# Optimization experiments

Measured on AMD Instinct MI355X. Metric: run time of the kernel, lower is better.

## Reference

```python
import jax, jax.numpy as jnp
import numpy as np

E, K, IN_DIM, OUT_DIM = 100000, 16, 128, 128


def _linear_init(key, out_d, in_d):
    kw, kb = jax.random.split(key)
    bound = 1.0 / np.sqrt(in_d)
    W = jax.random.uniform(kw, (out_d, in_d), minval=-bound, maxval=bound, dtype=jnp.float32)
    b = jax.random.uniform(kb, (out_d,), minval=-bound, maxval=bound, dtype=jnp.float32)
    return W, b


def setup_inputs() -> dict:
    key = jax.random.key(0)
    k_feat, k_adj, k1, k2, k3, k4 = jax.random.split(key, 6)
    edge_features = jax.random.normal(k_feat, (E, IN_DIM), dtype=jnp.float32)
    edge_adjacency = jax.random.randint(k_adj, (E, K), 0, E, dtype=jnp.int64)
    mW1, mb1 = _linear_init(k1, OUT_DIM, 2 * IN_DIM)
    mW2, mb2 = _linear_init(k2, OUT_DIM, OUT_DIM)
    uW1, ub1 = _linear_init(k3, OUT_DIM, IN_DIM + OUT_DIM)
    uW2, ub2 = _linear_init(k4, OUT_DIM, OUT_DIM)
    return {"edge_features": edge_features, "edge_adjacency": edge_adjacency,
            "mW1": mW1, "mb1": mb1, "mW2": mW2, "mb2": mb2,
            "uW1": uW1, "ub1": ub1, "uW2": ub2 * 0 + ub2 if False else uW1 * 0 + uW1 if False else uW1, "ub1_": ub1} if False else {
            "edge_features": edge_features, "edge_adjacency": edge_adjacency,
            "mW1": mW1, "mb1": mb1, "mW2": mW2, "mb2": mb2,
            "uW1": uW1, "ub1": ub1, "uW2": uW2, "ub2": ub2}


def reference(edge_features, edge_adjacency, mW1, mb1, mW2, mb2, uW1, ub1, uW2, ub2):
    D = edge_features.shape[1]
    # message_net first Linear on concat([feat_i, feat_j]) split into two halves
    # to avoid materializing the [E, K, 2D] concat tensor.
    Wi, Wj = mW1[:, :D], mW1[:, D:]                      # each [O, D]
    self_part = edge_features @ Wi.T                     # [E, O]
    nbr_feat = edge_features[edge_adjacency]             # [E, K, D] gather
    h = jax.nn.relu(self_part[:, None, :] + jnp.einsum('ekd,od->eko', nbr_feat, Wj) + mb1)
    msg = jnp.einsum('eko,po->ekp', h, mW2) + mb2        # [E, K, O]
    msg = msg.mean(axis=1)                               # mean over neighbors -> [E, O]
    # update_net on concat([feat_i, msg_i]), split likewise
    Ui, Um = uW1[:, :D], uW1[:, D:]
    u = jax.nn.relu(edge_features @ Ui.T + msg @ Um.T + ub1)
    return u @ uW2.T + ub2                               # [E, O]
```

## Files before the change

kernel.cpp:

```cpp
#include <hip/hip_runtime.h>
#include <hip/hip_bf16.h>

#define NE 100000
#define NK 16
#define ND 128
#define NTILES 6250

typedef __bf16 bf16_t;
typedef bf16_t bf16x8 __attribute__((ext_vector_type(8)));
typedef bf16_t bf16x4 __attribute__((ext_vector_type(4)));
typedef float f32x4 __attribute__((ext_vector_type(4)));
typedef float f32x2 __attribute__((ext_vector_type(2)));
typedef unsigned short u16;
typedef unsigned char u8;

__device__ __forceinline__ u16 f2bf(float f) {
  bf16_t h = (bf16_t)f;
  return __builtin_bit_cast(u16, h);
}

__global__ void k_prep(const float* __restrict__ mW1, const float* __restrict__ uW1,
                       const float* __restrict__ uW2, const float* __restrict__ mW2,
                       const float* __restrict__ ub1, const float* __restrict__ mb2,
                       u16* __restrict__ Wi_b, u16* __restrict__ Wj_b,
                       u16* __restrict__ Ui_b, u16* __restrict__ Wp_b,
                       u16* __restrict__ W2_b, float* __restrict__ bp)
{
  const int o = blockIdx.x, t = threadIdx.x;
  Wi_b[o * ND + t] = f2bf(mW1[o * 256 + t]);
  Wj_b[o * ND + t] = f2bf(mW1[o * 256 + 128 + t]);
  Ui_b[o * ND + t] = f2bf(uW1[o * 256 + t]);
  W2_b[o * ND + t] = f2bf(uW2[o * ND + t]);
  float acc = 0.f;
  for (int p = 0; p < 128; ++p)
    acc += uW1[o * 256 + 128 + p] * mW2[p * 128 + t];
  Wp_b[o * ND + t] = f2bf(acc);
  if (t == 0) {
    float b = ub1[o];
    for (int p = 0; p < 128; ++p) b += uW1[o * 256 + 128 + p] * mb2[p];
    bp[o] = b;
  }
}

__global__ __launch_bounds__(512) void k1_szt(
    const float* __restrict__ X, const u16* __restrict__ Wi_b,
    const u16* __restrict__ Wj_b, const u16* __restrict__ Ui_b,
    const float* __restrict__ mb1, const float* __restrict__ bp,
    u16* __restrict__ Sb, u8* __restrict__ Zf8, u16* __restrict__ T1)
{
  __shared__ u16 xt[16 * ND];
  __shared__ u16 eS[16 * ND];
  __shared__ u8  eZ[16 * ND];
  __shared__ u16 eT[16 * ND];
  const int tid = threadIdx.x, wid = tid >> 6, lane = tid & 63;
  const int r = lane & 15, q = lane >> 4;

  bf16x8 wiF[4], wjF[4], uiF[4];
  f32x4 mbF, bpF;
  {
    const int row = wid * 16 + r;
#pragma unroll
    for (int kk = 0; kk < 4; ++kk) {
      wiF[kk] = *(const bf16x8*)(Wi_b + row * ND + kk * 32 + q * 8);
      wjF[kk] = *(const bf16x8*)(Wj_b + row * ND + kk * 32 + q * 8);
      uiF[kk] = *(const bf16x8*)(Ui_b + row * ND + kk * 32 + q * 8);
    }
    mbF = *(const f32x4*)(mb1 + wid * 16 + q * 4);
    bpF = *(const f32x4*)(bp  + wid * 16 + q * 4);
  }

  const int rs = tid >> 5, cs = tid & 31;
  const int stb = rs * 256 + ((((cs >> 1) ^ (rs & 15)) << 4) | ((cs & 1) << 3));

  const int ewb = r * 256 + ((((wid * 2 + (q >> 1)) ^ (r & 15)) << 4) | ((q & 1) << 3));
  const int ezb = r * 128 + (((wid ^ (r & 7)) << 4) | (q * 4));
  const int erow = tid >> 5, c8 = tid & 31;
  const int erb = erow * 256 + ((((c8 >> 1) ^ (erow & 15)) << 4) | ((c8 & 1) << 3));
  const int zrb = erow * 128 + ((((c8 >> 2) ^ (erow & 7)) << 4) | ((c8 & 3) << 2));

  const long stride = gridDim.x;
  long t = blockIdx.x;
  if (t >= NTILES) return;

  f32x4 xr;
  auto gload = [&](long tt) {
    xr = *(const f32x4*)(X + (tt * 16 + rs) * ND + cs * 4);
  };
  auto stage = [&]() {
    bf16x4 b;
#pragma unroll
    for (int i = 0; i < 4; ++i) b[i] = (bf16_t)xr[i];
    *(bf16x4*)((char*)xt + stb) = b;
  };

  gload(t);
  stage();
  __syncthreads();

  for (; t < NTILES; t += stride) {
    const long tn = t + stride;
    if (tn < NTILES) gload(tn);

    bf16x8 xf[4];
#pragma unroll
    for (int kk = 0; kk < 4; ++kk)
      xf[kk] = *(const bf16x8*)((const char*)xt +
               r * 256 + (((kk * 4 + q) ^ (r & 15)) << 4));

    f32x4 aS = {0.f, 0.f, 0.f, 0.f};
    f32x4 aZ = {0.f, 0.f, 0.f, 0.f};
    f32x4 aT = {0.f, 0.f, 0.f, 0.f};
#pragma unroll
    for (int kk = 0; kk < 4; ++kk) {
      aS = __builtin_amdgcn_mfma_f32_16x16x32_bf16(wiF[kk], xf[kk], aS, 0, 0, 0);
      aZ = __builtin_amdgcn_mfma_f32_16x16x32_bf16(wjF[kk], xf[kk], aZ, 0, 0, 0);
      aT = __builtin_amdgcn_mfma_f32_16x16x32_bf16(uiF[kk], xf[kk], aT, 0, 0, 0);
    }

    bf16x4 pS, pT;
#pragma unroll
    for (int i = 0; i < 4; ++i) {
      pS[i] = (bf16_t)(aS[i] + mbF[i]);
      pT[i] = (bf16_t)(aT[i] + bpF[i]);
    }
    unsigned zpk = 0;
    zpk = __builtin_amdgcn_cvt_pk_fp8_f32(aZ[0], aZ[1], zpk, false);
    zpk = __builtin_amdgcn_cvt_pk_fp8_f32(aZ[2], aZ[3], zpk, true);
    *(bf16x4*)((char*)eS + ewb) = pS;
    *(bf16x4*)((char*)eT + ewb) = pT;
    *(unsigned*)((char*)eZ + ezb) = zpk;

    __syncthreads();

    {
      const long e = t * 16 + erow;
      const bf16x4 vS = *(const bf16x4*)((const char*)eS + erb);
      const bf16x4 vT = *(const bf16x4*)((const char*)eT + erb);
      const unsigned vZ = *(const unsigned*)((const char*)eZ + zrb);
      *(bf16x4*)(Sb + e * ND + c8 * 4) = vS;
      *(bf16x4*)(T1 + e * 256 + c8 * 4) = vT;
      *(unsigned*)(Zf8 + e * ND + c8 * 4) = vZ;
    }
    if (tn < NTILES) stage();

    __syncthreads();
  }
}

__global__ __launch_bounds__(256) void k2_gather(
    const u8* __restrict__ Zf8, const u16* __restrict__ Sb,
    const int* __restrict__ adj, u16* __restrict__ Hb)
{
  const int tid = threadIdx.x, w4 = tid >> 6, lane = tid & 63;
  const int sub = lane >> 5, l = lane & 31;
  const long e = (long)blockIdx.x * 8 + w4 * 2 + sub;
  const int c0 = l * 4;

  const bf16x4 sv = *(const bf16x4*)(Sb + e * ND + c0);
  f32x4 s;
#pragma unroll
  for (int i = 0; i < 4; ++i) s[i] = (float)sv[i];

  const int myidx = adj[e * NK + (lane & 15)];

  f32x4 acc = {0.f, 0.f, 0.f, 0.f};
#pragma unroll
  for (int k = 0; k < NK; ++k) {
    const int n = __shfl(myidx, (lane & 32) + k);
    const unsigned zw = *(const unsigned*)(Zf8 + (long)n * ND + c0);
    const f32x2 zlo = __builtin_amdgcn_cvt_pk_f32_fp8(zw, false);
    const f32x2 zhi = __builtin_amdgcn_cvt_pk_f32_fp8(zw, true);
    f32x4 z;
    z[0] = zlo[0]; z[1] = zlo[1]; z[2] = zhi[0]; z[3] = zhi[1];
    f32x4 v = s + z;
#pragma unroll
    for (int i = 0; i < 4; ++i) v[i] = fmaxf(v[i], 0.f);
    acc += v;
  }

  bf16x4 hv;
#pragma unroll
  for (int i = 0; i < 4; ++i) hv[i] = (bf16_t)(acc[i] * 0.0625f);
  *(bf16x4*)(Hb + e * ND + c0) = hv;
}

__global__ __launch_bounds__(512) void k3_out(
    const u16* __restrict__ Hb, const u16* __restrict__ T1,
    const u16* __restrict__ Wp_b, const u16* __restrict__ W2_b,
    const float* __restrict__ ub2, float* __restrict__ out)
{
  __shared__ u16 ht[16 * ND];
  __shared__ u16 ut[16 * ND];
  const int tid = threadIdx.x, wid = tid >> 6, lane = tid & 63;
  const int r = lane & 15, q = lane >> 4;

  bf16x8 wpF[4], w2F[4];
  f32x4 ubF;
  {
    const int row = wid * 16 + r;
#pragma unroll
    for (int kk = 0; kk < 4; ++kk) {
      wpF[kk] = *(const bf16x8*)(Wp_b + row * ND + kk * 32 + q * 8);
      w2F[kk] = *(const bf16x8*)(W2_b + row * ND + kk * 32 + q * 8);
    }
    ubF = *(const f32x4*)(ub2 + wid * 16 + q * 4);
  }

  const int rs = tid >> 5, cs = tid & 31;
  const int stb = rs * 256 + ((((cs >> 1) ^ (rs & 15)) << 4) | ((cs & 1) << 3));

  const long stride = gridDim.x;
  long t = blockIdx.x;
  if (t >= NTILES) return;

  bf16x4 hr;
  auto gload = [&](long tt) {
    hr = *(const bf16x4*)(Hb + (tt * 16 + rs) * ND + cs * 4);
  };
  gload(t);
  *(bf16x4*)((char*)ht + stb) = hr;
  __syncthreads();

  for (; t < NTILES; t += stride) {
    const long tn = t + stride;
    if (tn < NTILES) gload(tn);

    bf16x8 hf[4];
#pragma unroll
    for (int kk = 0; kk < 4; ++kk)
      hf[kk] = *(const bf16x8*)((const char*)ht +
               r * 256 + (((kk * 4 + q) ^ (r & 15)) << 4));

    f32x4 acc;
    {
      const bf16x4 tv = *(const bf16x4*)(T1 + (t * 16 + r) * 256 + wid * 16 + q * 4);
#pragma unroll
      for (int i = 0; i < 4; ++i) acc[i] = (float)tv[i];
    }
#pragma unroll
    for (int kk = 0; kk < 4; ++kk)
      acc = __builtin_amdgcn_mfma_f32_16x16x32_bf16(wpF[kk], hf[kk], acc, 0, 0, 0);

    bf16x4 u;
#pragma unroll
    for (int i = 0; i < 4; ++i) u[i] = (bf16_t)fmaxf(acc[i], 0.f);
    const int uwb = r * 256 + ((((wid * 2 + (q >> 1)) ^ (r & 15)) << 4) | ((q & 1) << 3));

    __syncthreads();
    *(bf16x4*)((char*)ut + uwb) = u;
    if (tn < NTILES) *(bf16x4*)((char*)ht + stb) = hr;
    __syncthreads();

    bf16x8 uf[4];
#pragma unroll
    for (int kk = 0; kk < 4; ++kk)
      uf[kk] = *(const bf16x8*)((const char*)ut +
               r * 256 + (((kk * 4 + q) ^ (r & 15)) << 4));

    f32x4 o = {0.f, 0.f, 0.f, 0.f};
#pragma unroll
    for (int kk = 0; kk < 4; ++kk)
      o = __builtin_amdgcn_mfma_f32_16x16x32_bf16(w2F[kk], uf[kk], o, 0, 0, 0);
#pragma unroll
    for (int i = 0; i < 4; ++i) o[i] += ubF[i];
    *(f32x4*)(out + (t * 16 + r) * ND + wid * 16 + q * 4) = o;
  }
}

extern "C" void kernel_launch(void* const* d_in, const int* in_sizes, int n_in,
                              void* d_out, int out_size, void* d_ws, size_t ws_size,
                              hipStream_t stream)
{
  (void)in_sizes; (void)n_in; (void)out_size; (void)ws_size;
  const float* X   = (const float*)d_in[0];
  const int*   adj = (const int*)d_in[1];
  const float* mW1 = (const float*)d_in[2];
  const float* mb1 = (const float*)d_in[3];
  const float* mW2 = (const float*)d_in[4];
  const float* mb2 = (const float*)d_in[5];
  const float* uW1 = (const float*)d_in[6];
  const float* ub1 = (const float*)d_in[7];
  const float* uW2 = (const float*)d_in[8];
  const float* ub2 = (const float*)d_in[9];
  float* out = (float*)d_out;

  u16* ws16 = (u16*)d_ws;
  u16* Sb   = ws16;
  u16* Hb   = Sb + (size_t)NE * ND;
  u8*  Zf8  = (u8*)(Hb + (size_t)NE * ND);
  u16* Wi_b = (u16*)(Zf8 + (size_t)NE * ND);
  u16* Wj_b = Wi_b + 128 * 128;
  u16* Ui_b = Wj_b + 128 * 128;
  u16* Wp_b = Ui_b + 128 * 128;
  u16* W2_b = Wp_b + 128 * 128;
  float* bp = (float*)(W2_b + 128 * 128);
  u16* T1   = (u16*)d_out;

  k_prep<<<128, 128, 0, stream>>>(mW1, uW1, uW2, mW2, ub1, mb2,
                                  Wi_b, Wj_b, Ui_b, Wp_b, W2_b, bp);

  k1_szt<<<1024, 512, 0, stream>>>(X, Wi_b, Wj_b, Ui_b, mb1, bp, Sb, Zf8, T1);

  k2_gather<<<NE / 8, 256, 0, stream>>>(Zf8, Sb, adj, Hb);

  k3_out<<<1024, 512, 0, stream>>>(Hb, T1, Wp_b, W2_b, ub2, out);
}
```

Before: 97.46 us.

## Double-buffer LDS tiles in k1 and drop the trailing barrier

```diff
diff --git a/kernel.cpp b/kernel.cpp
--- a/kernel.cpp
+++ b/kernel.cpp
@@ -48,10 +48,10 @@
     const float* __restrict__ mb1, const float* __restrict__ bp,
     u16* __restrict__ Sb, u8* __restrict__ Zf8, u16* __restrict__ T1)
 {
-  __shared__ u16 xt[16 * ND];
-  __shared__ u16 eS[16 * ND];
-  __shared__ u8  eZ[16 * ND];
-  __shared__ u16 eT[16 * ND];
+  __shared__ u16 xt[2][16 * ND];
+  __shared__ u16 eS[2][16 * ND];
+  __shared__ u8  eZ[2][16 * ND];
+  __shared__ u16 eT[2][16 * ND];
   const int tid = threadIdx.x, wid = tid >> 6, lane = tid & 63;
   const int r = lane & 15, q = lane >> 4;
 
@@ -71,7 +71,6 @@
 
   const int rs = tid >> 5, cs = tid & 31;
   const int stb = rs * 256 + ((((cs >> 1) ^ (rs & 15)) << 4) | ((cs & 1) << 3));
-
   const int ewb = r * 256 + ((((wid * 2 + (q >> 1)) ^ (r & 15)) << 4) | ((q & 1) << 3));
   const int ezb = r * 128 + (((wid ^ (r & 7)) << 4) | (q * 4));
   const int erow = tid >> 5, c8 = tid & 31;
@@ -86,26 +85,33 @@
   auto gload = [&](long tt) {
     xr = *(const f32x4*)(X + (tt * 16 + rs) * ND + cs * 4);
   };
-  auto stage = [&]() {
+  auto stage = [&](int bb) {
     bf16x4 b;
 #pragma unroll
     for (int i = 0; i < 4; ++i) b[i] = (bf16_t)xr[i];
-    *(bf16x4*)((char*)xt + stb) = b;
+    *(bf16x4*)((char*)xt[bb] + stb) = b;
   };
 
   gload(t);
-  stage();
+  stage(0);
+  {
+    const long t1 = t + stride;
+    if (t1 < NTILES) gload(t1);
+  }
   __syncthreads();
+  int b = 0;
 
   for (; t < NTILES; t += stride) {
-    const long tn = t + stride;
-    if (tn < NTILES) gload(tn);
+    const long tn = t + stride, tn2 = tn + stride;
 
     bf16x8 xf[4];
 #pragma unroll
     for (int kk = 0; kk < 4; ++kk)
-      xf[kk] = *(const bf16x8*)((const char*)xt +
+      xf[kk] = *(const bf16x8*)((const char*)xt[b] +
                r * 256 + (((kk * 4 + q) ^ (r & 15)) << 4));
+
+    if (tn < NTILES) stage(b ^ 1);
+    if (tn2 < NTILES) gload(tn2);
 
     f32x4 aS = {0.f, 0.f, 0.f, 0.f};
     f32x4 aZ = {0.f, 0.f, 0.f, 0.f};
@@ -126,24 +132,22 @@
     unsigned zpk = 0;
     zpk = __builtin_amdgcn_cvt_pk_fp8_f32(aZ[0], aZ[1], zpk, false);
     zpk = __builtin_amdgcn_cvt_pk_fp8_f32(aZ[2], aZ[3], zpk, true);
-    *(bf16x4*)((char*)eS + ewb) = pS;
-    *(bf16x4*)((char*)eT + ewb) = pT;
-    *(unsigned*)((char*)eZ + ezb) = zpk;
+    *(bf16x4*)((char*)eS[b] + ewb) = pS;
+    *(bf16x4*)((char*)eT[b] + ewb) = pT;
+    *(unsigned*)((char*)eZ[b] + ezb) = zpk;
 
     __syncthreads();
 
     {
       const long e = t * 16 + erow;
-      const bf16x4 vS = *(const bf16x4*)((const char*)eS + erb);
-      const bf16x4 vT = *(const bf16x4*)((const char*)eT + erb);
-      const unsigned vZ = *(const unsigned*)((const char*)eZ + zrb);
+      const bf16x4 vS = *(const bf16x4*)((const char*)eS[b] + erb);
+      const bf16x4 vT = *(const bf16x4*)((const char*)eT[b] + erb);
+      const unsigned vZ = *(const unsigned*)((const char*)eZ[b] + zrb);
       *(bf16x4*)(Sb + e * ND + c8 * 4) = vS;
       *(bf16x4*)(T1 + e * 256 + c8 * 4) = vT;
       *(unsigned*)(Zf8 + e * ND + c8 * 4) = vZ;
     }
-    if (tn < NTILES) stage();
-
-    __syncthreads();
+    b ^= 1;
   }
 }
 
```

Result: no change. 97.68 us (+0.2%).
